# Optimization experiments

Hardware: AMD Instinct MI355X
Metric: run time of the kernel (lower is better)

The kernel has to match this reference:

```python
import jax, jax.numpy as jnp
import numpy as np

DIM = 256
HEADS = 8
HEAD_DIM = DIM // HEADS


def setup_inputs() -> dict:
    key = jax.random.key(0)
    ks = jax.random.split(key, 10)
    B, Nq, Nk, C = 2, 2048, 2048, DIM
    inp = {
        "query": jax.random.normal(ks[0], (B, Nq, C), jnp.float32),
        "key": jax.random.normal(ks[1], (B, Nk, C), jnp.float32),
        "value": jax.random.normal(ks[2], (B, Nk, C), jnp.float32),
        "qpos": jnp.zeros((B, Nq), jnp.int32),
        "kpos": jnp.zeros((B, Nk), jnp.int32),
        "mask": jax.random.randint(ks[3], (Nq, Nk), 0, 2) > 0,
        "similarities": jax.random.normal(ks[4], (B, HEADS, Nq, Nk), jnp.float32),
        # learned params (torch Linear stored here as [C_in, C_out]; no qkv bias)
        "Wq": jax.random.normal(ks[5], (C, C), jnp.float32) / np.sqrt(C),
        "Wk": jax.random.normal(ks[6], (C, C), jnp.float32) / np.sqrt(C),
        "Wv": jax.random.normal(ks[7], (C, C), jnp.float32) / np.sqrt(C),
        "Wp": jax.random.normal(ks[8], (C, C), jnp.float32) / np.sqrt(C),
        "bp": jax.random.normal(ks[9], (C,), jnp.float32) * 0.01,
    }
    return inp


def reference(query, key, value, qpos, kpos, mask, similarities, Wq, Wk, Wv, Wp, bp):
    B, Nq, C = query.shape
    Nk = key.shape[1]
    H, hd = HEADS, HEAD_DIM
    scale = hd ** -0.5
    # projections -> [B, N, H, hd] (rope is None, so qpos/kpos are unused)
    q = (query @ Wq).reshape(B, Nq, H, hd)
    k = (key @ Wk).reshape(B, Nk, H, hd)
    v = (value @ Wv).reshape(B, Nk, H, hd)
    # scores [B, H, Nq, Nk]
    attn = jnp.einsum("bqhd,bkhd->bhqk", q, k) * scale
    # mean-centered similarity bias (mean over heads, dim=1)
    attn = attn + (similarities - similarities.mean(axis=1, keepdims=True))
    # boolean mask: fill False positions with -inf, then softmax over keys
    attn = jnp.where(mask[None, None, :, :], attn, -jnp.inf)
    attn = jax.nn.softmax(attn, axis=-1)
    # AV -> [B, Nq, C], output projection
    x = jnp.einsum("bhqk,bkhd->bqhd", attn, v).reshape(B, Nq, C)
    return x @ Wp + bp
```

## Files before the change

### kernel.cpp

```cpp
#include <hip/hip_runtime.h>

#define B_  2
#define NQ  2048
#define NK  2048
#define C_  256
#define H_  8
#define HD  32
#define SPLIT 4
#define KSEG (NK / SPLIT)
#define KT   (KSEG / 32)
#define QT_  (NQ / 16)
#define PART_STRIDE 544

typedef float f32x4 __attribute__((ext_vector_type(4)));
typedef __bf16 bf16x8 __attribute__((ext_vector_type(8)));
typedef unsigned short ushort8 __attribute__((ext_vector_type(8)));

static __device__ __forceinline__ unsigned short f2bf(float f) {
    unsigned int u = __builtin_bit_cast(unsigned int, f);
    u += 0x7FFFu + ((u >> 16) & 1u);
    return (unsigned short)(u >> 16);
}
static __device__ __forceinline__ float bf2f(unsigned short h) {
    unsigned int u = ((unsigned int)h) << 16;
    return __builtin_bit_cast(float, u);
}
static __device__ __forceinline__ unsigned int split1(float f) {
    unsigned short h = f2bf(f);
    unsigned short l = f2bf(f - bf2f(h));
    return (unsigned int)h | ((unsigned int)l << 16);
}
static __device__ __forceinline__ bf16x8 ld_bf16x8(const unsigned short* p) {
    return __builtin_bit_cast(bf16x8, *(const ushort8*)p);
}
static __device__ __forceinline__ void async16(const void* g, void* l) {
    __builtin_amdgcn_global_load_lds((__attribute__((address_space(1))) void*)g,
                                     (__attribute__((address_space(3))) void*)l,
                                     16, 0, 0);
}

__global__ __launch_bounds__(256) void maskpack_kernel(const int* __restrict__ mask,
                                                       unsigned short* __restrict__ mb)
{
    const int qt = blockIdx.x;
    const int k  = blockIdx.y * 256 + threadIdx.x;
    unsigned int m = 0;
    #pragma unroll
    for (int r = 0; r < 16; ++r)
        m |= (mask[(size_t)(qt * 16 + r) * NK + k] ? 1u : 0u) << r;
    mb[(size_t)qt * NK + k] = (unsigned short)m;
}

__global__ __launch_bounds__(256) void proj_kernel(
        const float* __restrict__ query, const float* __restrict__ key,
        const float* __restrict__ value,
        const float* __restrict__ Wq, const float* __restrict__ Wk,
        const float* __restrict__ Wv,
        unsigned short* __restrict__ qbh, unsigned short* __restrict__ qbl,
        unsigned short* __restrict__ kbh, unsigned short* __restrict__ kbl,
        unsigned short* __restrict__ vbh, unsigned short* __restrict__ vbl)
{
    __shared__ unsigned short WtH[64][40];
    __shared__ unsigned short WtL[64][40];

    const int z = blockIdx.z;
    const float* X = (z == 0) ? query : (z == 1) ? key : value;
    const float* W = (z == 0) ? Wq    : (z == 1) ? Wk  : Wv;
    unsigned short* dh = (z == 0) ? qbh : (z == 1) ? kbh : vbh;
    unsigned short* dl = (z == 0) ? qbl : (z == 1) ? kbl : vbl;
    const int vmode = (z == 2);

    const int tid  = threadIdx.x;
    const int wave = tid >> 6;
    const int lane = tid & 63;
    const int n15  = lane & 15;
    const int quad = lane >> 4;
    const int m0   = blockIdx.x * 64;
    const int j0   = blockIdx.y * 64;

    f32x4 acc[4];
    acc[0] = 0.f; acc[1] = 0.f; acc[2] = 0.f; acc[3] = 0.f;

    const int sj  = tid >> 2;
    const int skc = (tid & 3) * 8;
    const float* __restrict__ xrow = X + (size_t)(m0 + wave * 16 + n15) * C_;

    for (int k0 = 0; k0 < C_; k0 += 32) {
        ushort8 wh, wl;
        #pragma unroll
        for (int i = 0; i < 8; ++i) {
            unsigned int p = split1(W[(size_t)(k0 + skc + i) * C_ + j0 + sj]);
            wh[i] = (unsigned short)p;
            wl[i] = (unsigned short)(p >> 16);
        }
        *(ushort8*)&WtH[sj][skc] = wh;
        *(ushort8*)&WtL[sj][skc] = wl;
        __syncthreads();

        f32x4 a0 = *(const f32x4*)(xrow + k0 + quad * 8);
        f32x4 a1 = *(const f32x4*)(xrow + k0 + quad * 8 + 4);
        ushort8 ah, al;
        #pragma unroll
        for (int i = 0; i < 4; ++i) {
            unsigned int p0 = split1(a0[i]);
            unsigned int p1 = split1(a1[i]);
            ah[i]     = (unsigned short)p0;  al[i]     = (unsigned short)(p0 >> 16);
            ah[i + 4] = (unsigned short)p1;  al[i + 4] = (unsigned short)(p1 >> 16);
        }
        bf16x8 Ah = __builtin_bit_cast(bf16x8, ah);
        bf16x8 Al = __builtin_bit_cast(bf16x8, al);

        #pragma unroll
        for (int f = 0; f < 4; ++f) {
            bf16x8 Bh = ld_bf16x8(&WtH[f * 16 + n15][quad * 8]);
            bf16x8 Bl = ld_bf16x8(&WtL[f * 16 + n15][quad * 8]);
            acc[f] = __builtin_amdgcn_mfma_f32_16x16x32_bf16(Al, Bl, acc[f], 0, 0, 0);
            acc[f] = __builtin_amdgcn_mfma_f32_16x16x32_bf16(Al, Bh, acc[f], 0, 0, 0);
            acc[f] = __builtin_amdgcn_mfma_f32_16x16x32_bf16(Ah, Bl, acc[f], 0, 0, 0);
            acc[f] = __builtin_amdgcn_mfma_f32_16x16x32_bf16(Ah, Bh, acc[f], 0, 0, 0);
        }
        __syncthreads();
    }

    #pragma unroll
    for (int f = 0; f < 4; ++f) {
        const int j = j0 + f * 16 + n15;
        const int h = j >> 5, dd = j & 31;
        #pragma unroll
        for (int r = 0; r < 4; ++r) {
            const int grow = m0 + wave * 16 + quad * 4 + r;
            const int b = grow >> 11, row = grow & 2047;
            unsigned int p = split1(acc[f][r]);
            size_t idx;
            if (vmode) idx = (size_t)((b * H_ + h) * HD + dd) * NK + row;
            else       idx = (size_t)((b * H_ + h) * NK + row) * HD + dd;
            dh[idx] = (unsigned short)p;
            dl[idx] = (unsigned short)(p >> 16);
        }
    }
}

__global__ __launch_bounds__(256) void outproj_kernel(const unsigned short* __restrict__ Xh,
                                                      const unsigned short* __restrict__ Xl,
                                                      const float* __restrict__ W,
                                                      const float* __restrict__ bias,
                                                      float* __restrict__ out)
{
    __shared__ unsigned short WtH[64][40];
    __shared__ unsigned short WtL[64][40];

    const int tid  = threadIdx.x;
    const int wave = tid >> 6;
    const int lane = tid & 63;
    const int n15  = lane & 15;
    const int quad = lane >> 4;
    const int m0   = blockIdx.x * 64;
    const int j0   = blockIdx.y * 64;

    f32x4 acc[4];
    acc[0] = 0.f; acc[1] = 0.f; acc[2] = 0.f; acc[3] = 0.f;

    const int sj  = tid >> 2;
    const int skc = (tid & 3) * 8;
    const size_t xoff = (size_t)(m0 + wave * 16 + n15) * C_;

    for (int k0 = 0; k0 < C_; k0 += 32) {
        ushort8 wh, wl;
        #pragma unroll
        for (int i = 0; i < 8; ++i) {
            unsigned int p = split1(W[(size_t)(k0 + skc + i) * C_ + j0 + sj]);
            wh[i] = (unsigned short)p;
            wl[i] = (unsigned short)(p >> 16);
        }
        *(ushort8*)&WtH[sj][skc] = wh;
        *(ushort8*)&WtL[sj][skc] = wl;
        __syncthreads();

        bf16x8 Ah = ld_bf16x8(Xh + xoff + k0 + quad * 8);
        bf16x8 Al = ld_bf16x8(Xl + xoff + k0 + quad * 8);

        #pragma unroll
        for (int f = 0; f < 4; ++f) {
            bf16x8 Bh = ld_bf16x8(&WtH[f * 16 + n15][quad * 8]);
            bf16x8 Bl = ld_bf16x8(&WtL[f * 16 + n15][quad * 8]);
            acc[f] = __builtin_amdgcn_mfma_f32_16x16x32_bf16(Al, Bl, acc[f], 0, 0, 0);
            acc[f] = __builtin_amdgcn_mfma_f32_16x16x32_bf16(Al, Bh, acc[f], 0, 0, 0);
            acc[f] = __builtin_amdgcn_mfma_f32_16x16x32_bf16(Ah, Bl, acc[f], 0, 0, 0);
            acc[f] = __builtin_amdgcn_mfma_f32_16x16x32_bf16(Ah, Bh, acc[f], 0, 0, 0);
        }
        __syncthreads();
    }

    #pragma unroll
    for (int f = 0; f < 4; ++f) {
        const int j = j0 + f * 16 + n15;
        const float bj = bias[j];
        #pragma unroll
        for (int r = 0; r < 4; ++r) {
            const int grow = m0 + wave * 16 + quad * 4 + r;
            out[(size_t)grow * C_ + j] = acc[f][r] + bj;
        }
    }
}

__global__ __launch_bounds__(512, 6) void attn_kernel(
        const unsigned short* __restrict__ qh, const unsigned short* __restrict__ ql,
        const unsigned short* __restrict__ kh, const unsigned short* __restrict__ kl,
        const unsigned short* __restrict__ vh, const unsigned short* __restrict__ vl,
        const float* __restrict__ sim, const unsigned short* __restrict__ maskb,
        float* __restrict__ part)
{
    __shared__ __align__(16) float simLds[2][H_][16][32];
    __shared__ float biasLds[16][33];
    __shared__ __align__(16) unsigned short pLds[H_][16 * 40];

    const int tid  = threadIdx.x;
    const int wave = tid >> 6;
    const int lane = tid & 63;
    const int n15  = lane & 15;
    const int quad = lane >> 4;

    const int wg   = blockIdx.x;
    const int s    = wg >> 8;
    const int rem  = wg & 255;
    const int b    = rem >> 7;
    const int qt   = rem & 127;
    const int q0   = qt * 16;
    const int kbeg = s * KSEG;

    const size_t bh   = (size_t)(b * H_ + wave);
    const size_t qoff = (bh * NQ + q0 + n15) * HD + quad * 8;
    const unsigned short* khb = kh + bh * NK * HD;
    const unsigned short* klb = kl + bh * NK * HD;
    const unsigned short* vhb = vh + bh * HD * NK;
    const unsigned short* vlb = vl + bh * HD * NK;
    const unsigned short* mkb = maskb + (size_t)qt * NK + kbeg;
    const float* gsim = sim + (bh * NQ + q0 + (lane >> 3)) * (size_t)NK + kbeg
                            + (lane & 7) * 4;

    const bf16x8 Qh = ld_bf16x8(qh + qoff);
    const bf16x8 Ql = ld_bf16x8(ql + qoff);

    f32x4 O0 = 0.f, O1 = 0.f;
    float m_r[4] = {0.f, 0.f, 0.f, 0.f};
    float l_r[4] = {0.f, 0.f, 0.f, 0.f};

    const float scale = 0.17677669529663687f;
    const int kk = tid & 31;

    async16(gsim,                  &simLds[0][wave][0][0]);
    async16(gsim + (size_t)8 * NK, &simLds[0][wave][8][0]);
    unsigned short mcur = mkb[kk];

    for (int it = 0; it < KT; ++it) {
        const int k0  = kbeg + it * 32;
        const int cur = it & 1;
        const int last = (it == KT - 1);

        __syncthreads();

        {
            const int qq = tid >> 5;
            float sum = 0.f;
            #pragma unroll
            for (int h = 0; h < H_; ++h) sum += simLds[cur][h][qq][kk];
            biasLds[qq][kk] = ((mcur >> qq) & 1) ? (-0.125f * sum) : -1e30f;
        }
        __syncthreads();

        const size_t koA = (size_t)(k0 + n15) * HD + quad * 8;
        const size_t koB = (size_t)(k0 + 16 + n15) * HD + quad * 8;
        bf16x8 Kh0 = ld_bf16x8(khb + koA), Kl0 = ld_bf16x8(klb + koA);
        bf16x8 Kh1 = ld_bf16x8(khb + koB), Kl1 = ld_bf16x8(klb + koB);
        const size_t voA = (size_t)n15 * NK + k0 + quad * 8;
        const size_t voB = (size_t)(16 + n15) * NK + k0 + quad * 8;
        bf16x8 Vh0 = ld_bf16x8(vhb + voA), Vl0 = ld_bf16x8(vlb + voA);
        bf16x8 Vh1 = ld_bf16x8(vhb + voB), Vl1 = ld_bf16x8(vlb + voB);
        if (!last) mcur = mkb[(it + 1) * 32 + kk];

        if (!last) {
            __builtin_amdgcn_sched_barrier(0);
            const float* g = gsim + it * 32 + 32;
            async16(g,                  &simLds[cur ^ 1][wave][0][0]);
            async16(g + (size_t)8 * NK, &simLds[cur ^ 1][wave][8][0]);
            __builtin_amdgcn_sched_barrier(0);
        }

        f32x4 S0 = 0.f, S1 = 0.f;
        S0 = __builtin_amdgcn_mfma_f32_16x16x32_bf16(Ql, Kl0, S0, 0, 0, 0);
        S0 = __builtin_amdgcn_mfma_f32_16x16x32_bf16(Ql, Kh0, S0, 0, 0, 0);
        S0 = __builtin_amdgcn_mfma_f32_16x16x32_bf16(Qh, Kl0, S0, 0, 0, 0);
        S0 = __builtin_amdgcn_mfma_f32_16x16x32_bf16(Qh, Kh0, S0, 0, 0, 0);
        S1 = __builtin_amdgcn_mfma_f32_16x16x32_bf16(Ql, Kl1, S1, 0, 0, 0);
        S1 = __builtin_amdgcn_mfma_f32_16x16x32_bf16(Ql, Kh1, S1, 0, 0, 0);
        S1 = __builtin_amdgcn_mfma_f32_16x16x32_bf16(Qh, Kl1, S1, 0, 0, 0);
        S1 = __builtin_amdgcn_mfma_f32_16x16x32_bf16(Qh, Kh1, S1, 0, 0, 0);

        unsigned int u0[4], u1[4];
        #pragma unroll
        for (int r = 0; r < 4; ++r) {
            const int qq = quad * 4 + r;
            float s0 = S0[r] * scale + simLds[cur][wave][qq][n15]      + biasLds[qq][n15];
            float s1 = S1[r] * scale + simLds[cur][wave][qq][16 + n15] + biasLds[qq][16 + n15];

            float mx = fmaxf(s0, s1);
            #pragma unroll
            for (int off = 1; off < 16; off <<= 1) mx = fmaxf(mx, __shfl_xor(mx, off));
            const float mnew = fmaxf(m_r[r], mx);
            const float a  = __expf(m_r[r] - mnew);
            const float p0 = __expf(s0 - mnew);
            const float p1 = __expf(s1 - mnew);
            float sm = p0 + p1;
            #pragma unroll
            for (int off = 1; off < 16; off <<= 1) sm += __shfl_xor(sm, off);
            l_r[r] = l_r[r] * a + sm;
            m_r[r] = mnew;
            O0[r] *= a; O1[r] *= a;
            u0[r] = split1(p0); u1[r] = split1(p1);
        }

        unsigned short* pw = pLds[wave];
        #pragma unroll
        for (int r = 0; r < 4; ++r) {
            const int qq = quad * 4 + r;
            pw[qq * 40 + n15]      = (unsigned short)u0[r];
            pw[qq * 40 + 16 + n15] = (unsigned short)u1[r];
        }
        bf16x8 Ph = ld_bf16x8(pw + n15 * 40 + quad * 8);
        #pragma unroll
        for (int r = 0; r < 4; ++r) {
            const int qq = quad * 4 + r;
            pw[qq * 40 + n15]      = (unsigned short)(u0[r] >> 16);
            pw[qq * 40 + 16 + n15] = (unsigned short)(u1[r] >> 16);
        }
        bf16x8 Pl = ld_bf16x8(pw + n15 * 40 + quad * 8);

        O0 = __builtin_amdgcn_mfma_f32_16x16x32_bf16(Pl, Vl0, O0, 0, 0, 0);
        O0 = __builtin_amdgcn_mfma_f32_16x16x32_bf16(Pl, Vh0, O0, 0, 0, 0);
        O0 = __builtin_amdgcn_mfma_f32_16x16x32_bf16(Ph, Vl0, O0, 0, 0, 0);
        O0 = __builtin_amdgcn_mfma_f32_16x16x32_bf16(Ph, Vh0, O0, 0, 0, 0);
        O1 = __builtin_amdgcn_mfma_f32_16x16x32_bf16(Pl, Vl1, O1, 0, 0, 0);
        O1 = __builtin_amdgcn_mfma_f32_16x16x32_bf16(Pl, Vh1, O1, 0, 0, 0);
        O1 = __builtin_amdgcn_mfma_f32_16x16x32_bf16(Ph, Vl1, O1, 0, 0, 0);
        O1 = __builtin_amdgcn_mfma_f32_16x16x32_bf16(Ph, Vh1, O1, 0, 0, 0);
    }

    float* pb = part + (size_t)(((s * B_ + b) * H_ + wave) * QT_ + qt) * PART_STRIDE;
    #pragma unroll
    for (int r = 0; r < 4; ++r) {
        const int q = quad * 4 + r;
        pb[q * 32 + n15]      = O0[r];
        pb[q * 32 + 16 + n15] = O1[r];
        if (n15 == 0) {
            pb[512 + q] = m_r[r];
            pb[528 + q] = l_r[r];
        }
    }
}

__global__ __launch_bounds__(256) void combine_kernel(const float* __restrict__ part,
                                                      unsigned short* __restrict__ xh,
                                                      unsigned short* __restrict__ xl)
{
    const int wid  = blockIdx.x * 4 + (threadIdx.x >> 6);
    const int lane = threadIdx.x & 63;
    const int b  = wid >> 10;
    const int h  = (wid >> 7) & 7;
    const int qt = wid & 127;
    const int q  = lane >> 2;
    const int d0 = (lane & 3) * 8;

    float ms[SPLIT], ls[SPLIT];
    float mstar = -1e30f;
    #pragma unroll
    for (int s = 0; s < SPLIT; ++s) {
        const float* pb = part + (size_t)(((s * B_ + b) * H_ + h) * QT_ + qt) * PART_STRIDE;
        ms[s] = pb[512 + q];
        ls[s] = pb[528 + q];
        mstar = fmaxf(mstar, ms[s]);
    }
    f32x4 acc0 = 0.f, acc1 = 0.f;
    float lsum = 0.f;
    #pragma unroll
    for (int s = 0; s < SPLIT; ++s) {
        const float* pb = part + (size_t)(((s * B_ + b) * H_ + h) * QT_ + qt) * PART_STRIDE;
        const float w = __expf(ms[s] - mstar);
        lsum += w * ls[s];
        f32x4 o0 = *(const f32x4*)(pb + q * 32 + d0);
        f32x4 o1 = *(const f32x4*)(pb + q * 32 + d0 + 4);
        acc0 += w * o0;
        acc1 += w * o1;
    }
    const float inv = 1.0f / lsum;
    const size_t base = (size_t)(b * NQ + qt * 16 + q) * C_ + h * HD + d0;
    #pragma unroll
    for (int i = 0; i < 4; ++i) {
        unsigned int p0 = split1(acc0[i] * inv);
        unsigned int p1 = split1(acc1[i] * inv);
        xh[base + i]     = (unsigned short)p0;
        xl[base + i]     = (unsigned short)(p0 >> 16);
        xh[base + 4 + i] = (unsigned short)p1;
        xl[base + 4 + i] = (unsigned short)(p1 >> 16);
    }
}

extern "C" void kernel_launch(void* const* d_in, const int* in_sizes, int n_in,
                              void* d_out, int out_size, void* d_ws, size_t ws_size,
                              hipStream_t stream) {
    const float* query = (const float*)d_in[0];
    const float* key   = (const float*)d_in[1];
    const float* value = (const float*)d_in[2];
    const int*   mask  = (const int*)d_in[5];
    const float* sim   = (const float*)d_in[6];
    const float* Wq  = (const float*)d_in[7];
    const float* Wk  = (const float*)d_in[8];
    const float* Wv  = (const float*)d_in[9];
    const float* Wp  = (const float*)d_in[10];
    const float* bp  = (const float*)d_in[11];
    float* out = (float*)d_out;

    const size_t NEL = (size_t)B_ * H_ * NQ * HD;
    unsigned short* qbh = (unsigned short*)d_ws;
    unsigned short* qbl = qbh + NEL;
    unsigned short* kbh = qbl + NEL;
    unsigned short* kbl = kbh + NEL;
    unsigned short* vbh = kbl + NEL;
    unsigned short* vbl = vbh + NEL;
    unsigned short* xbh = vbl + NEL;
    unsigned short* xbl = xbh + NEL;
    float* part = (float*)(xbl + NEL);
    unsigned short* maskbW = (unsigned short*)(part
                            + (size_t)SPLIT * B_ * H_ * QT_ * PART_STRIDE);

    maskpack_kernel<<<dim3(QT_, NK / 256), 256, 0, stream>>>(mask, maskbW);
    proj_kernel<<<dim3(64, 4, 3), 256, 0, stream>>>(query, key, value, Wq, Wk, Wv,
                                                    qbh, qbl, kbh, kbl, vbh, vbl);
    attn_kernel<<<SPLIT * 256, 512, 0, stream>>>(qbh, qbl, kbh, kbl, vbh, vbl,
                                                 sim, maskbW, part);
    combine_kernel<<<512, 256, 0, stream>>>(part, xbh, xbl);
    outproj_kernel<<<dim3(64, 4), 256, 0, stream>>>(xbh, xbl, Wp, bp, out);
}
```

Baseline: 643.2 us.

## Register-prefetch similarity tiles, use lighter LDS barriers, and reorder block mapping

Replaces the async global-to-LDS loads of the similarity tile with register prefetch. The next tile's loads are issued early and written into the alternate LDS buffer at the end of each iteration. __syncthreads is replaced with an LDS-only waitcnt plus s_barrier, so the barrier does not wait on outstanding global loads. The last iteration is peeled, V loads move after the QK MFMAs, the sim LDS rows are padded to 33, and the block index mapping is changed so the split/batch blocks of one q-tile run adjacently and share mask/sim locality. The aim is to hide global-load latency behind compute and avoid full-vmcnt waits at barriers, at the cost of more registers and a duplicated loop tail.

```diff
diff --git a/kernel.cpp b/kernel.cpp
--- a/kernel.cpp
+++ b/kernel.cpp
@@ -33,10 +33,12 @@
 static __device__ __forceinline__ bf16x8 ld_bf16x8(const unsigned short* p) {
     return __builtin_bit_cast(bf16x8, *(const ushort8*)p);
 }
-static __device__ __forceinline__ void async16(const void* g, void* l) {
-    __builtin_amdgcn_global_load_lds((__attribute__((address_space(1))) void*)g,
-                                     (__attribute__((address_space(3))) void*)l,
-                                     16, 0, 0);
+
+static __device__ __forceinline__ void barrier_lds() {
+    __builtin_amdgcn_sched_barrier(0);
+    asm volatile("s_waitcnt lgkmcnt(0)" ::: "memory");
+    __builtin_amdgcn_s_barrier();
+    __builtin_amdgcn_sched_barrier(0);
 }
 
 __global__ __launch_bounds__(256) void maskpack_kernel(const int* __restrict__ mask,
@@ -210,7 +212,7 @@
         const float* __restrict__ sim, const unsigned short* __restrict__ maskb,
         float* __restrict__ part)
 {
-    __shared__ __align__(16) float simLds[2][H_][16][32];
+    __shared__ __align__(16) float simLds[2][H_][16][33];
     __shared__ float biasLds[16][33];
     __shared__ __align__(16) unsigned short pLds[H_][16 * 40];
 
@@ -220,12 +222,12 @@
     const int n15  = lane & 15;
     const int quad = lane >> 4;
 
-    const int wg   = blockIdx.x;
-    const int s    = wg >> 8;
-    const int rem  = wg & 255;
-    const int b    = rem >> 7;
-    const int qt   = rem & 127;
-    const int q0   = qt * 16;
+    const int wg = blockIdx.x;
+    const int qt = wg >> 3;
+    const int sb = wg & 7;
+    const int s  = sb >> 1;
+    const int b  = sb & 1;
+    const int q0 = qt * 16;
     const int kbeg = s * KSEG;
 
     const size_t bh   = (size_t)(b * H_ + wave);
@@ -235,8 +237,10 @@
     const unsigned short* vhb = vh + bh * HD * NK;
     const unsigned short* vlb = vl + bh * HD * NK;
     const unsigned short* mkb = maskb + (size_t)qt * NK + kbeg;
-    const float* gsim = sim + (bh * NQ + q0 + (lane >> 3)) * (size_t)NK + kbeg
-                            + (lane & 7) * 4;
+
+    const int swr = lane >> 2, swc = (lane & 3) * 8;
+    const float* gsim = sim + (bh * NQ + q0 + swr) * (size_t)NK + kbeg + swc;
+    const int kk = tid & 31;
 
     const bf16x8 Qh = ld_bf16x8(qh + qoff);
     const bf16x8 Ql = ld_bf16x8(ql + qoff);
@@ -246,18 +250,31 @@
     float l_r[4] = {0.f, 0.f, 0.f, 0.f};
 
     const float scale = 0.17677669529663687f;
-    const int kk = tid & 31;
-
-    async16(gsim,                  &simLds[0][wave][0][0]);
-    async16(gsim + (size_t)8 * NK, &simLds[0][wave][8][0]);
+
+    {
+        f32x4 pA = *(const f32x4*)gsim;
+        f32x4 pB = *(const f32x4*)(gsim + 4);
+        float* sw0 = &simLds[0][wave][swr][swc];
+        *(f32x4*)sw0       = pA;
+        *(f32x4*)(sw0 + 4) = pB;
+    }
     unsigned short mcur = mkb[kk];
 
-    for (int it = 0; it < KT; ++it) {
+    for (int it = 0; it < KT - 1; ++it) {
         const int k0  = kbeg + it * 32;
         const int cur = it & 1;
-        const int last = (it == KT - 1);
-
-        __syncthreads();
+
+        const size_t koA = (size_t)(k0 + n15) * HD + quad * 8;
+        const size_t koB = (size_t)(k0 + 16 + n15) * HD + quad * 8;
+        bf16x8 Kh0 = ld_bf16x8(khb + koA), Kl0 = ld_bf16x8(klb + koA);
+        bf16x8 Kh1 = ld_bf16x8(khb + koB), Kl1 = ld_bf16x8(klb + koB);
+        const unsigned short mnext = mkb[(it + 1) * 32 + kk];
+        __builtin_amdgcn_sched_barrier(0);
+        f32x4 nA = *(const f32x4*)(gsim + (it + 1) * 32);
+        f32x4 nB = *(const f32x4*)(gsim + (it + 1) * 32 + 4);
+        __builtin_amdgcn_sched_barrier(0);
+
+        barrier_lds();
 
         {
             const int qq = tid >> 5;
@@ -266,25 +283,7 @@
             for (int h = 0; h < H_; ++h) sum += simLds[cur][h][qq][kk];
             biasLds[qq][kk] = ((mcur >> qq) & 1) ? (-0.125f * sum) : -1e30f;
         }
-        __syncthreads();
-
-        const size_t koA = (size_t)(k0 + n15) * HD + quad * 8;
-        const size_t koB = (size_t)(k0 + 16 + n15) * HD + quad * 8;
-        bf16x8 Kh0 = ld_bf16x8(khb + koA), Kl0 = ld_bf16x8(klb + koA);
-        bf16x8 Kh1 = ld_bf16x8(khb + koB), Kl1 = ld_bf16x8(klb + koB);
-        const size_t voA = (size_t)n15 * NK + k0 + quad * 8;
-        const size_t voB = (size_t)(16 + n15) * NK + k0 + quad * 8;
-        bf16x8 Vh0 = ld_bf16x8(vhb + voA), Vl0 = ld_bf16x8(vlb + voA);
-        bf16x8 Vh1 = ld_bf16x8(vhb + voB), Vl1 = ld_bf16x8(vlb + voB);
-        if (!last) mcur = mkb[(it + 1) * 32 + kk];
-
-        if (!last) {
-            __builtin_amdgcn_sched_barrier(0);
-            const float* g = gsim + it * 32 + 32;
-            async16(g,                  &simLds[cur ^ 1][wave][0][0]);
-            async16(g + (size_t)8 * NK, &simLds[cur ^ 1][wave][8][0]);
-            __builtin_amdgcn_sched_barrier(0);
-        }
+        barrier_lds();
 
         f32x4 S0 = 0.f, S1 = 0.f;
         S0 = __builtin_amdgcn_mfma_f32_16x16x32_bf16(Ql, Kl0, S0, 0, 0, 0);
@@ -295,6 +294,11 @@
         S1 = __builtin_amdgcn_mfma_f32_16x16x32_bf16(Ql, Kh1, S1, 0, 0, 0);
         S1 = __builtin_amdgcn_mfma_f32_16x16x32_bf16(Qh, Kl1, S1, 0, 0, 0);
         S1 = __builtin_amdgcn_mfma_f32_16x16x32_bf16(Qh, Kh1, S1, 0, 0, 0);
+
+        const size_t voA = (size_t)n15 * NK + k0 + quad * 8;
+        const size_t voB = (size_t)(16 + n15) * NK + k0 + quad * 8;
+        bf16x8 Vh0 = ld_bf16x8(vhb + voA), Vl0 = ld_bf16x8(vlb + voA);
+        bf16x8 Vh1 = ld_bf16x8(vhb + voB), Vl1 = ld_bf16x8(vlb + voB);
 
         unsigned int u0[4], u1[4];
         #pragma unroll
@@ -343,6 +347,95 @@
         O1 = __builtin_amdgcn_mfma_f32_16x16x32_bf16(Pl, Vh1, O1, 0, 0, 0);
         O1 = __builtin_amdgcn_mfma_f32_16x16x32_bf16(Ph, Vl1, O1, 0, 0, 0);
         O1 = __builtin_amdgcn_mfma_f32_16x16x32_bf16(Ph, Vh1, O1, 0, 0, 0);
+
+        float* swn = &simLds[cur ^ 1][wave][swr][swc];
+        *(f32x4*)swn       = nA;
+        *(f32x4*)(swn + 4) = nB;
+        mcur = mnext;
+    }
+
+    {
+        const int it = KT - 1;
+        const int k0 = kbeg + it * 32;
+        const int cur = it & 1;
+
+        const size_t koA = (size_t)(k0 + n15) * HD + quad * 8;
+        const size_t koB = (size_t)(k0 + 16 + n15) * HD + quad * 8;
+        bf16x8 Kh0 = ld_bf16x8(khb + koA), Kl0 = ld_bf16x8(klb + koA);
+        bf16x8 Kh1 = ld_bf16x8(khb + koB), Kl1 = ld_bf16x8(klb + koB);
+
+        barrier_lds();
+        {
+            const int qq = tid >> 5;
+            float sum = 0.f;
+            #pragma unroll
+            for (int h = 0; h < H_; ++h) sum += simLds[cur][h][qq][kk];
+            biasLds[qq][kk] = ((mcur >> qq) & 1) ? (-0.125f * sum) : -1e30f;
+        }
+        barrier_lds();
+
+        f32x4 S0 = 0.f, S1 = 0.f;
+        S0 = __builtin_amdgcn_mfma_f32_16x16x32_bf16(Ql, Kl0, S0, 0, 0, 0);
+        S0 = __builtin_amdgcn_mfma_f32_16x16x32_bf16(Ql, Kh0, S0, 0, 0, 0);
+        S0 = __builtin_amdgcn_mfma_f32_16x16x32_bf16(Qh, Kl0, S0, 0, 0, 0);
+        S0 = __builtin_amdgcn_mfma_f32_16x16x32_bf16(Qh, Kh0, S0, 0, 0, 0);
+        S1 = __builtin_amdgcn_mfma_f32_16x16x32_bf16(Ql, Kl1, S1, 0, 0, 0);
+        S1 = __builtin_amdgcn_mfma_f32_16x16x32_bf16(Ql, Kh1, S1, 0, 0, 0);
+        S1 = __builtin_amdgcn_mfma_f32_16x16x32_bf16(Qh, Kl1, S1, 0, 0, 0);
+        S1 = __builtin_amdgcn_mfma_f32_16x16x32_bf16(Qh, Kh1, S1, 0, 0, 0);
+
+        const size_t voA = (size_t)n15 * NK + k0 + quad * 8;
+        const size_t voB = (size_t)(16 + n15) * NK + k0 + quad * 8;
+        bf16x8 Vh0 = ld_bf16x8(vhb + voA), Vl0 = ld_bf16x8(vlb + voA);
+        bf16x8 Vh1 = ld_bf16x8(vhb + voB), Vl1 = ld_bf16x8(vlb + voB);
+
+        unsigned int u0[4], u1[4];
+        #pragma unroll
+        for (int r = 0; r < 4; ++r) {
+            const int qq = quad * 4 + r;
+            float s0 = S0[r] * scale + simLds[cur][wave][qq][n15]      + biasLds[qq][n15];
+            float s1 = S1[r] * scale + simLds[cur][wave][qq][16 + n15] + biasLds[qq][16 + n15];
+
+            float mx = fmaxf(s0, s1);
+            #pragma unroll
+            for (int off = 1; off < 16; off <<= 1) mx = fmaxf(mx, __shfl_xor(mx, off));
+            const float mnew = fmaxf(m_r[r], mx);
+            const float a  = __expf(m_r[r] - mnew);
+            const float p0 = __expf(s0 - mnew);
+            const float p1 = __expf(s1 - mnew);
+            float sm = p0 + p1;
+            #pragma unroll
+            for (int off = 1; off < 16; off <<= 1) sm += __shfl_xor(sm, off);
+            l_r[r] = l_r[r] * a + sm;
+            m_r[r] = mnew;
+            O0[r] *= a; O1[r] *= a;
+            u0[r] = split1(p0); u1[r] = split1(p1);
+        }
+
+        unsigned short* pw = pLds[wave];
+        #pragma unroll
+        for (int r = 0; r < 4; ++r) {
+            const int qq = quad * 4 + r;
+            pw[qq * 40 + n15]      = (unsigned short)u0[r];
+            pw[qq * 40 + 16 + n15] = (unsigned short)u1[r];
+        }
+        bf16x8 Ph = ld_bf16x8(pw + n15 * 40 + quad * 8);
+        #pragma unroll
+        for (int r = 0; r < 4; ++r) {
+            const int qq = quad * 4 + r;
+            pw[qq * 40 + n15]      = (unsigned short)(u0[r] >> 16);
+            pw[qq * 40 + 16 + n15] = (unsigned short)(u1[r] >> 16);
+        }
+        bf16x8 Pl = ld_bf16x8(pw + n15 * 40 + quad * 8);
+
+        O0 = __builtin_amdgcn_mfma_f32_16x16x32_bf16(Pl, Vl0, O0, 0, 0, 0);
+        O0 = __builtin_amdgcn_mfma_f32_16x16x32_bf16(Pl, Vh0, O0, 0, 0, 0);
+        O0 = __builtin_amdgcn_mfma_f32_16x16x32_bf16(Ph, Vl0, O0, 0, 0, 0);
+        O0 = __builtin_amdgcn_mfma_f32_16x16x32_bf16(Ph, Vh0, O0, 0, 0, 0);
+        O1 = __builtin_amdgcn_mfma_f32_16x16x32_bf16(Pl, Vl1, O1, 0, 0, 0);
+        O1 = __builtin_amdgcn_mfma_f32_16x16x32_bf16(Pl, Vh1, O1, 0, 0, 0);
+        O1 = __builtin_amdgcn_mfma_f32_16x16x32_bf16(Ph, Vl1, O1, 0, 0, 0);
+        O1 = __builtin_amdgcn_mfma_f32_16x16x32_bf16(Ph, Vh1, O1, 0, 0, 0);
     }
 
     float* pb = part + (size_t)(((s * B_ + b) * H_ + wave) * QT_ + qt) * PART_STRIDE;
```

Result: slower. 735.9 us (+14.4%).

## Prefetch similarity tiles through registers, stage mask in LDS, coalesce V stores

Applied to the files above, without the earlier changes.

In the attention kernel, the similarity tiles are no longer loaded with async global-to-LDS copies. They are now prefetched into registers one tile ahead and written into a padded LDS buffer after the AV MFMAs. The 16-bit mask words for the whole key segment are preloaded into LDS once. V loads move after the softmax, and the block barriers wait only on lgkmcnt, so the aim is better overlap of memory latency with compute. The projection kernel now transposes V through LDS so the transposed output is written as coalesced 16-byte stores instead of scattered 2-byte stores. Risks: the 16-byte vector stores into rows padded to 33 floats are misaligned, and LDS use grows.

```diff
diff --git a/kernel.cpp b/kernel.cpp
--- a/kernel.cpp
+++ b/kernel.cpp
@@ -33,10 +33,12 @@
 static __device__ __forceinline__ bf16x8 ld_bf16x8(const unsigned short* p) {
     return __builtin_bit_cast(bf16x8, *(const ushort8*)p);
 }
-static __device__ __forceinline__ void async16(const void* g, void* l) {
-    __builtin_amdgcn_global_load_lds((__attribute__((address_space(1))) void*)g,
-                                     (__attribute__((address_space(3))) void*)l,
-                                     16, 0, 0);
+
+static __device__ __forceinline__ void barrier_lds() {
+    __builtin_amdgcn_sched_barrier(0);
+    asm volatile("s_waitcnt lgkmcnt(0)" ::: "memory");
+    __builtin_amdgcn_s_barrier();
+    __builtin_amdgcn_sched_barrier(0);
 }
 
 __global__ __launch_bounds__(256) void maskpack_kernel(const int* __restrict__ mask,
@@ -62,6 +64,8 @@
 {
     __shared__ unsigned short WtH[64][40];
     __shared__ unsigned short WtL[64][40];
+    __shared__ unsigned short TrH[64][80];
+    __shared__ unsigned short TrL[64][80];
 
     const int z = blockIdx.z;
     const float* X = (z == 0) ? query : (z == 1) ? key : value;
@@ -122,20 +126,42 @@
         __syncthreads();
     }
 
-    #pragma unroll
-    for (int f = 0; f < 4; ++f) {
-        const int j = j0 + f * 16 + n15;
-        const int h = j >> 5, dd = j & 31;
-        #pragma unroll
-        for (int r = 0; r < 4; ++r) {
-            const int grow = m0 + wave * 16 + quad * 4 + r;
-            const int b = grow >> 11, row = grow & 2047;
-            unsigned int p = split1(acc[f][r]);
-            size_t idx;
-            if (vmode) idx = (size_t)((b * H_ + h) * HD + dd) * NK + row;
-            else       idx = (size_t)((b * H_ + h) * NK + row) * HD + dd;
-            dh[idx] = (unsigned short)p;
-            dl[idx] = (unsigned short)(p >> 16);
+    if (vmode) {
+        #pragma unroll
+        for (int f = 0; f < 4; ++f) {
+            const int jl = f * 16 + n15;
+            #pragma unroll
+            for (int r = 0; r < 4; ++r) {
+                const int rowl = wave * 16 + quad * 4 + r;
+                unsigned int p = split1(acc[f][r]);
+                TrH[jl][rowl] = (unsigned short)p;
+                TrL[jl][rowl] = (unsigned short)(p >> 16);
+            }
+        }
+        __syncthreads();
+        const int jl = tid >> 2, chunk = (tid & 3) * 16;
+        const int j  = j0 + jl, h = j >> 5, dd = j & 31;
+        const int bb = m0 >> 11;
+        const size_t obase = (size_t)((bb * H_ + h) * HD + dd) * NK
+                           + (m0 & 2047) + chunk;
+        *(ushort8*)(dh + obase)     = *(const ushort8*)&TrH[jl][chunk];
+        *(ushort8*)(dh + obase + 8) = *(const ushort8*)&TrH[jl][chunk + 8];
+        *(ushort8*)(dl + obase)     = *(const ushort8*)&TrL[jl][chunk];
+        *(ushort8*)(dl + obase + 8) = *(const ushort8*)&TrL[jl][chunk + 8];
+    } else {
+        #pragma unroll
+        for (int f = 0; f < 4; ++f) {
+            const int j = j0 + f * 16 + n15;
+            const int h = j >> 5, dd = j & 31;
+            #pragma unroll
+            for (int r = 0; r < 4; ++r) {
+                const int grow = m0 + wave * 16 + quad * 4 + r;
+                const int b = grow >> 11, row = grow & 2047;
+                unsigned int p = split1(acc[f][r]);
+                size_t idx = (size_t)((b * H_ + h) * NK + row) * HD + dd;
+                dh[idx] = (unsigned short)p;
+                dl[idx] = (unsigned short)(p >> 16);
+            }
         }
     }
 }
@@ -210,9 +236,10 @@
         const float* __restrict__ sim, const unsigned short* __restrict__ maskb,
         float* __restrict__ part)
 {
-    __shared__ __align__(16) float simLds[2][H_][16][32];
+    __shared__ __align__(16) float simLds[2][H_][16][33];
     __shared__ float biasLds[16][33];
     __shared__ __align__(16) unsigned short pLds[H_][16 * 40];
+    __shared__ unsigned short maskLds[KSEG];
 
     const int tid  = threadIdx.x;
     const int wave = tid >> 6;
@@ -235,8 +262,10 @@
     const unsigned short* vhb = vh + bh * HD * NK;
     const unsigned short* vlb = vl + bh * HD * NK;
     const unsigned short* mkb = maskb + (size_t)qt * NK + kbeg;
-    const float* gsim = sim + (bh * NQ + q0 + (lane >> 3)) * (size_t)NK + kbeg
-                            + (lane & 7) * 4;
+
+    const int swr = lane >> 2, swc = (lane & 3) * 8;
+    const float* gsim = sim + (bh * NQ + q0 + swr) * (size_t)NK + kbeg + swc;
+    const int kk = tid & 31;
 
     const bf16x8 Qh = ld_bf16x8(qh + qoff);
     const bf16x8 Ql = ld_bf16x8(ql + qoff);
@@ -246,45 +275,43 @@
     float l_r[4] = {0.f, 0.f, 0.f, 0.f};
 
     const float scale = 0.17677669529663687f;
-    const int kk = tid & 31;
-
-    async16(gsim,                  &simLds[0][wave][0][0]);
-    async16(gsim + (size_t)8 * NK, &simLds[0][wave][8][0]);
-    unsigned short mcur = mkb[kk];
-
-    for (int it = 0; it < KT; ++it) {
+
+    maskLds[tid] = mkb[tid];
+    {
+        f32x4 pA = *(const f32x4*)gsim;
+        f32x4 pB = *(const f32x4*)(gsim + 4);
+        float* sw0 = &simLds[0][wave][swr][swc];
+        *(f32x4*)sw0       = pA;
+        *(f32x4*)(sw0 + 4) = pB;
+    }
+
+    auto tile_body = [&](int it, bool pf) {
+        const int cur = it & 1;
         const int k0  = kbeg + it * 32;
-        const int cur = it & 1;
-        const int last = (it == KT - 1);
-
-        __syncthreads();
+
+        barrier_lds();
 
         {
             const int qq = tid >> 5;
             float sum = 0.f;
             #pragma unroll
             for (int h = 0; h < H_; ++h) sum += simLds[cur][h][qq][kk];
-            biasLds[qq][kk] = ((mcur >> qq) & 1) ? (-0.125f * sum) : -1e30f;
-        }
-        __syncthreads();
+            const unsigned short mw = maskLds[it * 32 + kk];
+            biasLds[qq][kk] = ((mw >> qq) & 1) ? (-0.125f * sum) : -1e30f;
+        }
+        barrier_lds();
 
         const size_t koA = (size_t)(k0 + n15) * HD + quad * 8;
         const size_t koB = (size_t)(k0 + 16 + n15) * HD + quad * 8;
         bf16x8 Kh0 = ld_bf16x8(khb + koA), Kl0 = ld_bf16x8(klb + koA);
         bf16x8 Kh1 = ld_bf16x8(khb + koB), Kl1 = ld_bf16x8(klb + koB);
-        const size_t voA = (size_t)n15 * NK + k0 + quad * 8;
-        const size_t voB = (size_t)(16 + n15) * NK + k0 + quad * 8;
-        bf16x8 Vh0 = ld_bf16x8(vhb + voA), Vl0 = ld_bf16x8(vlb + voA);
-        bf16x8 Vh1 = ld_bf16x8(vhb + voB), Vl1 = ld_bf16x8(vlb + voB);
-        if (!last) mcur = mkb[(it + 1) * 32 + kk];
-
-        if (!last) {
-            __builtin_amdgcn_sched_barrier(0);
-            const float* g = gsim + it * 32 + 32;
-            async16(g,                  &simLds[cur ^ 1][wave][0][0]);
-            async16(g + (size_t)8 * NK, &simLds[cur ^ 1][wave][8][0]);
-            __builtin_amdgcn_sched_barrier(0);
-        }
+        __builtin_amdgcn_sched_barrier(0);
+        f32x4 nA, nB;
+        if (pf) {
+            nA = *(const f32x4*)(gsim + (it + 1) * 32);
+            nB = *(const f32x4*)(gsim + (it + 1) * 32 + 4);
+        }
+        __builtin_amdgcn_sched_barrier(0);
 
         f32x4 S0 = 0.f, S1 = 0.f;
         S0 = __builtin_amdgcn_mfma_f32_16x16x32_bf16(Ql, Kl0, S0, 0, 0, 0);
@@ -319,6 +346,13 @@
             u0[r] = split1(p0); u1[r] = split1(p1);
         }
 
+        __builtin_amdgcn_sched_barrier(0);
+        const size_t voA = (size_t)n15 * NK + k0 + quad * 8;
+        const size_t voB = (size_t)(16 + n15) * NK + k0 + quad * 8;
+        bf16x8 Vh0 = ld_bf16x8(vhb + voA), Vl0 = ld_bf16x8(vlb + voA);
+        bf16x8 Vh1 = ld_bf16x8(vhb + voB), Vl1 = ld_bf16x8(vlb + voB);
+        __builtin_amdgcn_sched_barrier(0);
+
         unsigned short* pw = pLds[wave];
         #pragma unroll
         for (int r = 0; r < 4; ++r) {
@@ -343,7 +377,16 @@
         O1 = __builtin_amdgcn_mfma_f32_16x16x32_bf16(Pl, Vh1, O1, 0, 0, 0);
         O1 = __builtin_amdgcn_mfma_f32_16x16x32_bf16(Ph, Vl1, O1, 0, 0, 0);
         O1 = __builtin_amdgcn_mfma_f32_16x16x32_bf16(Ph, Vh1, O1, 0, 0, 0);
-    }
+
+        if (pf) {
+            float* swn = &simLds[cur ^ 1][wave][swr][swc];
+            *(f32x4*)swn       = nA;
+            *(f32x4*)(swn + 4) = nB;
+        }
+    };
+
+    for (int it = 0; it < KT - 1; ++it) tile_body(it, true);
+    tile_body(KT - 1, false);
 
     float* pb = part + (size_t)(((s * B_ + b) * H_ + wave) * QT_ + qt) * PART_STRIDE;
     #pragma unroll
```

Measured after the change: 606.5 us. -5.7%, faster.
